# Kernel optimization log

Hardware: AMD Instinct MI355X
Metric: run time of the kernel (lower is better)

The kernel has to match this reference:

```python
import jax, jax.numpy as jnp
import numpy as np
import math

B, C_IN, C_QK, H, W, NH = 1, 256, 128, 96, 96, 8
SCALE = math.sqrt(C_QK / NH)  # sqrt(planes/num_head) = 4.0
TEMP = 1.0


def conv1x1(x, w, b=None):
    # x: [B, Cin, H, W], w: [Cout, Cin] -> [B, Cout, H, W]
    y = jnp.einsum('bchw,oc->bohw', x, w)
    if b is not None:
        y = y + b[None, :, None, None]
    return y


def maxpool2x2(x):
    return jax.lax.reduce_window(x, -jnp.inf, jax.lax.max,
                                 (1, 1, 2, 2), (1, 1, 2, 2), 'VALID')


def setup_inputs() -> dict:
    key = jax.random.key(0)
    ks = jax.random.split(key, 5)
    x = jax.random.normal(ks[0], (B, C_IN, H, W), dtype=jnp.float32)
    # conv weights: init.normal_(w, 0, 0.01), zero bias; conv_value has no bias
    w_q = jax.random.normal(ks[1], (C_QK, C_IN), dtype=jnp.float32) * 0.01
    b_q = jnp.zeros((C_QK,), dtype=jnp.float32)
    w_k = jax.random.normal(ks[2], (C_QK, C_IN), dtype=jnp.float32) * 0.01
    b_k = jnp.zeros((C_QK,), dtype=jnp.float32)
    w_v = jax.random.normal(ks[3], (C_IN, C_IN), dtype=jnp.float32) * 0.01
    return {'x': x, 'w_q': w_q, 'b_q': b_q, 'w_k': w_k, 'b_k': b_k, 'w_v': w_v}


def reference(x, w_q, b_q, w_k, b_k, w_v):
    residual = x
    input_x = maxpool2x2(x)                       # [B, Cin, H/2, W/2]
    Hd, Wd = H // 2, W // 2
    Nq, Nk = H * W, Hd * Wd

    q = conv1x1(x, w_q, b_q)                      # [B, Cqk, H, W]
    k = conv1x1(input_x, w_k, b_k)                # [B, Cqk, Hd, Wd]
    v = conv1x1(input_x, w_v)                     # [B, Cin, Hd, Wd]

    dq = C_QK // NH
    dv = C_IN // NH
    q = q.reshape(B * NH, dq, Nq)
    k = k.reshape(B * NH, dq, Nk)
    v = v.reshape(B * NH, dv, Nk)

    # dot distance: scaled by sqrt(planes/num_head) and temp (nowd empty)
    sim = jnp.einsum('bdq,bdk->bqk', q, k) / (SCALE * TEMP)
    attn = jax.nn.softmax(sim, axis=2)            # softmax over keys

    # out = value @ attn^T  -> [B*NH, dv, Nq]
    out = jnp.einsum('bdk,bqk->bdq', v, attn)
    out = out.reshape(B, C_IN, H, W)
    return out + residual
```

## Files before the change

kernel.cpp:

```cpp
#include <hip/hip_runtime.h>
#include <hip/hip_bf16.h>
#include <math.h>

#define C_IN   256
#define C_QK   128
#define NH     8
#define H_     96
#define W_     96
#define NQ     (H_*W_)
#define HD     48
#define WD     48
#define NK     (HD*WD)
#define DQ     16
#define DV     32
#define NQC    (NQ/32)
#define NKC    (NK/32)
#define KSTEPS (C_IN/16)
#define QS     0.3606737602222409f

typedef __attribute__((ext_vector_type(8)))  short short8v;
typedef __attribute__((ext_vector_type(16))) float f32x16;
typedef __attribute__((ext_vector_type(2)))  int   v2i;

union B8u { uint u[4]; short8v v; };

static __device__ inline ushort bf16r(float f) {
    __hip_bfloat16 h = __float2bfloat16(f);
    return *reinterpret_cast<ushort*>(&h);
}
static __device__ inline uint cvtpk(float lo, float hi) {
    uint r;
    asm("v_cvt_pk_bf16_f32 %0, %1, %2" : "=v"(r) : "v"(lo), "v"(hi));
    return r;
}
static __device__ inline void lswap(uint a, uint b, uint& x, uint& y, int hi) {
#if __has_builtin(__builtin_amdgcn_permlane32_swap)
    v2i r = __builtin_amdgcn_permlane32_swap((int)a, (int)b, false, false);
    x = (uint)r.x;
    y = (uint)r.y;
#else
    uint bx = (uint)__shfl_xor((int)b, 32);
    uint ax = (uint)__shfl_xor((int)a, 32);
    x = hi ? bx : a;
    y = hi ? b : ax;
#endif
}
static __device__ inline float fexp2(float v) {
#if __has_builtin(__builtin_amdgcn_exp2f)
    return __builtin_amdgcn_exp2f(v);
#else
    return __expf(v * 0.6931471805599453f);
#endif
}

#define U_XB   (NQC*KSTEPS*64)
#define U_XPB  (NKC*KSTEPS*64)
#define U_WQ   (4*KSTEPS*64)
#define U_WK   (4*KSTEPS*64)
#define U_WV   (8*KSTEPS*64)
#define U_FRAG (U_XB+U_XPB+U_WQ+U_WK+U_WV)
#define U_TOT  (U_FRAG + 128)

__global__ __launch_bounds__(256) void prep_kernel(
    const float* __restrict__ x,  const float* __restrict__ wq, const float* __restrict__ bq,
    const float* __restrict__ wk, const float* __restrict__ wv,
    ushort* __restrict__ xbP, ushort* __restrict__ xpbP,
    ushort* __restrict__ wqP, ushort* __restrict__ wkP, ushort* __restrict__ wvP,
    float* __restrict__ bqs)
{
    int t = blockIdx.x * 256 + threadIdx.x;
    if (t >= U_TOT) return;
    if (t >= U_FRAG) { int i = t - U_FRAG; bqs[i] = bq[i] * QS; return; }

    union { ushort s[8]; uint4 v; } ou;
    int u = t;
    if (u < U_XB) {
        int l = u & 63, rest = u >> 6;
        int ks = rest & 15, nc = rest >> 4;
        int n  = nc * 32 + (l & 31);
        int k0 = ks * 16 + 8 * (l >> 5);
        #pragma unroll
        for (int j = 0; j < 8; ++j) ou.s[j] = bf16r(x[(size_t)(k0 + j) * NQ + n]);
        *(uint4*)&xbP[(size_t)u * 8] = ou.v;
        return;
    }
    u -= U_XB;
    if (u < U_XPB) {
        int l = u & 63, rest = u >> 6;
        int ks = rest & 15, nc = rest >> 4;
        int np = nc * 32 + (l & 31);
        int k0 = ks * 16 + 8 * (l >> 5);
        int py = np / WD, px = np - py * WD;
        const float* base = x + (2 * py) * W_ + 2 * px;
        #pragma unroll
        for (int j = 0; j < 8; ++j) {
            const float* p = base + (size_t)(k0 + j) * NQ;
            ou.s[j] = bf16r(fmaxf(fmaxf(p[0], p[1]), fmaxf(p[W_], p[W_ + 1])));
        }
        *(uint4*)&xpbP[(size_t)u * 8] = ou.v;
        return;
    }
    u -= U_XPB;
    if (u < U_WQ) {
        int l = u & 63, ks = (u >> 6) & 15, mb = u >> 10;
        int m = mb * 32 + (l & 31), k0 = ks * 16 + 8 * (l >> 5);
        #pragma unroll
        for (int j = 0; j < 8; ++j) ou.s[j] = bf16r(wq[m * C_IN + k0 + j] * QS);
        *(uint4*)&wqP[(size_t)u * 8] = ou.v;
        return;
    }
    u -= U_WQ;
    if (u < U_WK) {
        int l = u & 63, ks = (u >> 6) & 15, mb = u >> 10;
        int m = mb * 32 + (l & 31), k0 = ks * 16 + 8 * (l >> 5);
        #pragma unroll
        for (int j = 0; j < 8; ++j) ou.s[j] = bf16r(wk[m * C_IN + k0 + j]);
        *(uint4*)&wkP[(size_t)u * 8] = ou.v;
        return;
    }
    u -= U_WK;
    {
        int l = u & 63, ks = (u >> 6) & 15, cb = u >> 10;
        int c = cb * 32 + (l & 31), k0 = ks * 16 + 8 * (l >> 5);
        #pragma unroll
        for (int j = 0; j < 8; ++j) ou.s[j] = bf16r(wv[c * C_IN + k0 + j]);
        *(uint4*)&wvP[(size_t)u * 8] = ou.v;
    }
}

static __device__ inline f32x16 mfma_loop(const ushort* __restrict__ A,
                                          const ushort* __restrict__ B) {
    f32x16 acc;
    #pragma unroll
    for (int r = 0; r < 16; ++r) acc[r] = 0.0f;
    #pragma unroll
    for (int s = 0; s < KSTEPS; ++s) {
        short8v a = *(const short8v*)(A + (size_t)s * 512);
        short8v b = *(const short8v*)(B + (size_t)s * 512);
        acc = __builtin_amdgcn_mfma_f32_32x32x16_bf16(a, b, acc, 0, 0, 0);
    }
    return acc;
}
static __device__ inline void xform(const f32x16& acc, int hi, short8v& F1, short8v& F2) {
    uint a0 = cvtpk(acc[0],  acc[1]),  a1 = cvtpk(acc[2],  acc[3]);
    uint b0 = cvtpk(acc[4],  acc[5]),  b1 = cvtpk(acc[6],  acc[7]);
    uint a2 = cvtpk(acc[8],  acc[9]),  a3 = cvtpk(acc[10], acc[11]);
    uint b2 = cvtpk(acc[12], acc[13]), b3 = cvtpk(acc[14], acc[15]);
    B8u f1, f2;
    lswap(a0, b0, f1.u[0], f1.u[2], hi);
    lswap(a1, b1, f1.u[1], f1.u[3], hi);
    lswap(a2, b2, f2.u[0], f2.u[2], hi);
    lswap(a3, b3, f2.u[1], f2.u[3], hi);
    F1 = f1.v; F2 = f2.v;
}

__global__ __launch_bounds__(256) void gemm_qk(const ushort* __restrict__ Wp,
                                               const ushort* __restrict__ Xp,
                                               const float* __restrict__ bias,
                                               ushort* __restrict__ outP, int NC) {
    int lane = threadIdx.x & 63, wvi = threadIdx.x >> 6;
    int hi = lane >> 5;
    int mb = blockIdx.x;
    int nc = blockIdx.y * 4 + wvi;
    const ushort* A = Wp + ((size_t)(mb * KSTEPS) * 64 + lane) * 8;
    const ushort* B = Xp + ((size_t)(nc * KSTEPS) * 64 + lane) * 8;
    f32x16 acc = mfma_loop(A, B);
    #pragma unroll
    for (int r = 0; r < 16; ++r)
        acc[r] += bias[mb * 32 + (r & 3) + 8 * (r >> 2) + 4 * hi];
    short8v F1, F2;
    xform(acc, hi, F1, F2);
    *(short8v*)&outP[((size_t)((2 * mb)     * NC + nc) * 64 + lane) * 8] = F1;
    *(short8v*)&outP[((size_t)((2 * mb + 1) * NC + nc) * 64 + lane) * 8] = F2;
}

__global__ __launch_bounds__(256) void gemm_v(const ushort* __restrict__ Xp,
                                              const ushort* __restrict__ Wvp,
                                              ushort* __restrict__ vpack) {
    int lane = threadIdx.x & 63, wvi = threadIdx.x >> 6;
    int hi = lane >> 5;
    int cb = blockIdx.x;
    int kc = blockIdx.y * 4 + wvi;
    const ushort* A = Xp  + ((size_t)(kc * KSTEPS) * 64 + lane) * 8;
    const ushort* B = Wvp + ((size_t)(cb * KSTEPS) * 64 + lane) * 8;
    f32x16 acc = mfma_loop(A, B);
    short8v F1, F2;
    xform(acc, hi, F1, F2);
    *(short8v*)&vpack[((size_t)((cb * NKC + kc) * 2 + 0) * 64 + lane) * 8] = F1;
    *(short8v*)&vpack[((size_t)((cb * NKC + kc) * 2 + 1) * 64 + lane) * 8] = F2;
}

__global__ __launch_bounds__(256) void attn_kernel(const ushort* __restrict__ qpack,
                                                   const ushort* __restrict__ kpack,
                                                   const ushort* __restrict__ vpack,
                                                   const float* __restrict__ x,
                                                   float* __restrict__ out) {
    __shared__ float comb[2 * 64 * 17];
    const int h = blockIdx.y;
    const int tid = threadIdx.x, lane = tid & 63;
    const int wvi = tid >> 6;
    const int qg = wvi & 1, kh = wvi >> 1;
    const int q31 = lane & 31, hi = lane >> 5;
    const int qc = blockIdx.x * 2 + qg;
    const int q = qc * 32 + q31;

    short8v qf = *(const short8v*)&qpack[((size_t)(h * NQC + qc) * 64 + lane) * 8];

    const ushort* kp = kpack + ((size_t)(h * NKC + kh * 36) * 64 + lane) * 8;
    const ushort* vp = vpack + ((size_t)(h * NKC + kh * 36) * 2 * 64 + lane) * 8;

    short8v kf = *(const short8v*)kp;
    short8v v0 = *(const short8v*)vp;
    short8v v1 = *(const short8v*)(vp + 512);

    f32x16 o, zc;
    #pragma unroll
    for (int r = 0; r < 16; ++r) { o[r] = 0.0f; zc[r] = 0.0f; }
    float rsum = 0.0f;

    #pragma unroll 2
    for (int c = 0; c < 36; ++c) {
        short8v kcur = kf, v0c = v0, v1c = v1;
        int cn = (c == 35) ? 0 : (c + 1);
        kf = *(const short8v*)(kp + (size_t)cn * 512);
        v0 = *(const short8v*)(vp + (size_t)cn * 1024);
        v1 = *(const short8v*)(vp + (size_t)cn * 1024 + 512);

        f32x16 s = __builtin_amdgcn_mfma_f32_32x32x16_bf16(kcur, qf, zc, 0, 0, 0);

        float e[16];
        #pragma unroll
        for (int r = 0; r < 16; ++r) e[r] = fexp2(s[r]);
        float t0 = 0.0f;
        #pragma unroll
        for (int r = 0; r < 16; ++r) t0 += e[r];
        rsum += t0;

        uint a0 = cvtpk(e[0],  e[1]),  a1 = cvtpk(e[2],  e[3]);
        uint b0 = cvtpk(e[4],  e[5]),  b1 = cvtpk(e[6],  e[7]);
        uint a2 = cvtpk(e[8],  e[9]),  a3 = cvtpk(e[10], e[11]);
        uint b2 = cvtpk(e[12], e[13]), b3 = cvtpk(e[14], e[15]);
        B8u B1, B2;
        lswap(a0, b0, B1.u[0], B1.u[2], hi);
        lswap(a1, b1, B1.u[1], B1.u[3], hi);
        lswap(a2, b2, B2.u[0], B2.u[2], hi);
        lswap(a3, b3, B2.u[1], B2.u[3], hi);

        o = __builtin_amdgcn_mfma_f32_32x32x16_bf16(v0c, B1.v, o, 0, 0, 0);
        o = __builtin_amdgcn_mfma_f32_32x32x16_bf16(v1c, B2.v, o, 0, 0, 0);
    }

    rsum += __shfl_xor(rsum, 32);

    if (kh == 1) {
        float* cb_ = &comb[(qg * 64 + lane) * 17];
        #pragma unroll
        for (int r = 0; r < 16; ++r) cb_[r] = o[r];
        cb_[16] = rsum;
    }
    __syncthreads();
    if (kh == 0) {
        const float* cb_ = &comb[(qg * 64 + lane) * 17];
        #pragma unroll
        for (int r = 0; r < 16; ++r) o[r] += cb_[r];
        float inv = 1.0f / (rsum + cb_[16]);
        #pragma unroll
        for (int r = 0; r < 16; ++r) {
            int dv = (r & 3) + 8 * (r >> 2) + 4 * hi;
            size_t i0 = (size_t)(h * DV + dv) * NQ + q;
            out[i0] = o[r] * inv + x[i0];
        }
    }
}

extern "C" void kernel_launch(void* const* d_in, const int* in_sizes, int n_in,
                              void* d_out, int out_size, void* d_ws, size_t ws_size,
                              hipStream_t stream) {
    const float* x  = (const float*)d_in[0];
    const float* wq = (const float*)d_in[1];
    const float* bq = (const float*)d_in[2];
    const float* wk = (const float*)d_in[3];
    const float* bk = (const float*)d_in[4];
    const float* wv = (const float*)d_in[5];
    float* out = (float*)d_out;

    ushort* p = (ushort*)d_ws;
    ushort* xbP   = p;  p += (size_t)U_XB  * 8;
    ushort* xpbP  = p;  p += (size_t)U_XPB * 8;
    ushort* wqP   = p;  p += (size_t)U_WQ  * 8;
    ushort* wkP   = p;  p += (size_t)U_WK  * 8;
    ushort* wvP   = p;  p += (size_t)U_WV  * 8;
    ushort* qpack = p;  p += (size_t)NH * NQC * 64 * 8;
    ushort* kpack = p;  p += (size_t)NH * NKC * 64 * 8;
    ushort* vpack = p;  p += (size_t)NH * NKC * 2 * 64 * 8;
    float*  bqs   = (float*)p;

    prep_kernel<<<(U_TOT + 255) / 256, 256, 0, stream>>>(x, wq, bq, wk, wv,
                                                         xbP, xpbP, wqP, wkP, wvP, bqs);
    gemm_qk<<<dim3(4, NQC / 4), 256, 0, stream>>>(wqP, xbP, bqs, qpack, NQC);
    gemm_qk<<<dim3(4, NKC / 4), 256, 0, stream>>>(wkP, xpbP, bk, kpack, NKC);
    gemm_v <<<dim3(NH, NKC / 4), 256, 0, stream>>>(xpbP, wvP, vpack);
    attn_kernel<<<dim3(NQC / 2, NH), 256, 0, stream>>>(qpack, kpack, vpack, x, out);
}
```

Baseline: 118.0 us.

## Fuse projection GEMMs into one launch and split attention keys four ways

The three separate projection GEMM launches (Q, K, V) are merged into one kernel that maps a flat tile index to the right sub-GEMM, which removes two launch gaps and lets the small K/V work share the machine with Q. The attention kernel now has each wave handle two query chunks against a quarter of the keys, so each K/V fragment load is reused across two queries. Partial outputs and row sums from all four waves are combined through shared memory. This costs more registers (launch bound of 4 blocks per SM hint) and a larger reduction step, and the grid keeps the same number of blocks.

```diff
diff --git a/kernel.cpp b/kernel.cpp
--- a/kernel.cpp
+++ b/kernel.cpp
@@ -15,6 +15,8 @@
 #define DV     32
 #define NQC    (NQ/32)
 #define NKC    (NK/32)
+#define QPAIRS (NQC/2)
+#define KQRT   (NKC/4)
 #define KSTEPS (C_IN/16)
 #define QS     0.3606737602222409f
 
@@ -154,116 +156,171 @@
     F1 = f1.v; F2 = f2.v;
 }
 
-__global__ __launch_bounds__(256) void gemm_qk(const ushort* __restrict__ Wp,
-                                               const ushort* __restrict__ Xp,
-                                               const float* __restrict__ bias,
-                                               ushort* __restrict__ outP, int NC) {
+#define T_Q 1152
+#define T_K (T_Q + 288)
+#define T_ALL (T_K + 576)
+
+__global__ __launch_bounds__(256) void gemm_fused(
+    const ushort* __restrict__ xbP, const ushort* __restrict__ xpbP,
+    const ushort* __restrict__ wqP, const ushort* __restrict__ wkP,
+    const ushort* __restrict__ wvP,
+    const float* __restrict__ bqs, const float* __restrict__ bk,
+    ushort* __restrict__ qpack, ushort* __restrict__ kpack, ushort* __restrict__ vpack)
+{
     int lane = threadIdx.x & 63, wvi = threadIdx.x >> 6;
     int hi = lane >> 5;
-    int mb = blockIdx.x;
-    int nc = blockIdx.y * 4 + wvi;
-    const ushort* A = Wp + ((size_t)(mb * KSTEPS) * 64 + lane) * 8;
-    const ushort* B = Xp + ((size_t)(nc * KSTEPS) * 64 + lane) * 8;
-    f32x16 acc = mfma_loop(A, B);
-    #pragma unroll
-    for (int r = 0; r < 16; ++r)
-        acc[r] += bias[mb * 32 + (r & 3) + 8 * (r >> 2) + 4 * hi];
-    short8v F1, F2;
-    xform(acc, hi, F1, F2);
-    *(short8v*)&outP[((size_t)((2 * mb)     * NC + nc) * 64 + lane) * 8] = F1;
-    *(short8v*)&outP[((size_t)((2 * mb + 1) * NC + nc) * 64 + lane) * 8] = F2;
-}
-
-__global__ __launch_bounds__(256) void gemm_v(const ushort* __restrict__ Xp,
-                                              const ushort* __restrict__ Wvp,
-                                              ushort* __restrict__ vpack) {
-    int lane = threadIdx.x & 63, wvi = threadIdx.x >> 6;
-    int hi = lane >> 5;
-    int cb = blockIdx.x;
-    int kc = blockIdx.y * 4 + wvi;
-    const ushort* A = Xp  + ((size_t)(kc * KSTEPS) * 64 + lane) * 8;
-    const ushort* B = Wvp + ((size_t)(cb * KSTEPS) * 64 + lane) * 8;
-    f32x16 acc = mfma_loop(A, B);
-    short8v F1, F2;
-    xform(acc, hi, F1, F2);
-    *(short8v*)&vpack[((size_t)((cb * NKC + kc) * 2 + 0) * 64 + lane) * 8] = F1;
-    *(short8v*)&vpack[((size_t)((cb * NKC + kc) * 2 + 1) * 64 + lane) * 8] = F2;
-}
-
-__global__ __launch_bounds__(256) void attn_kernel(const ushort* __restrict__ qpack,
-                                                   const ushort* __restrict__ kpack,
-                                                   const ushort* __restrict__ vpack,
-                                                   const float* __restrict__ x,
-                                                   float* __restrict__ out) {
-    __shared__ float comb[2 * 64 * 17];
+    int t = blockIdx.x * 4 + wvi;
+    if (t >= T_ALL) return;
+
+    if (t < T_Q) {
+        int mb = t / NQC, nc = t - mb * NQC;
+        const ushort* A = wqP + ((size_t)(mb * KSTEPS) * 64 + lane) * 8;
+        const ushort* B = xbP + ((size_t)(nc * KSTEPS) * 64 + lane) * 8;
+        f32x16 acc = mfma_loop(A, B);
+        #pragma unroll
+        for (int r = 0; r < 16; ++r)
+            acc[r] += bqs[mb * 32 + (r & 3) + 8 * (r >> 2) + 4 * hi];
+        short8v F1, F2;
+        xform(acc, hi, F1, F2);
+        *(short8v*)&qpack[((size_t)((2 * mb)     * NQC + nc) * 64 + lane) * 8] = F1;
+        *(short8v*)&qpack[((size_t)((2 * mb + 1) * NQC + nc) * 64 + lane) * 8] = F2;
+    } else if (t < T_K) {
+        int t2 = t - T_Q;
+        int mb = t2 / NKC, nc = t2 - mb * NKC;
+        const ushort* A = wkP  + ((size_t)(mb * KSTEPS) * 64 + lane) * 8;
+        const ushort* B = xpbP + ((size_t)(nc * KSTEPS) * 64 + lane) * 8;
+        f32x16 acc = mfma_loop(A, B);
+        #pragma unroll
+        for (int r = 0; r < 16; ++r)
+            acc[r] += bk[mb * 32 + (r & 3) + 8 * (r >> 2) + 4 * hi];
+        short8v F1, F2;
+        xform(acc, hi, F1, F2);
+        *(short8v*)&kpack[((size_t)((2 * mb)     * NKC + nc) * 64 + lane) * 8] = F1;
+        *(short8v*)&kpack[((size_t)((2 * mb + 1) * NKC + nc) * 64 + lane) * 8] = F2;
+    } else {
+        int t3 = t - T_K;
+        int cb = t3 / NKC, kc = t3 - cb * NKC;
+        const ushort* A = xpbP + ((size_t)(kc * KSTEPS) * 64 + lane) * 8;
+        const ushort* B = wvP  + ((size_t)(cb * KSTEPS) * 64 + lane) * 8;
+        f32x16 acc = mfma_loop(A, B);
+        short8v F1, F2;
+        xform(acc, hi, F1, F2);
+        *(short8v*)&vpack[((size_t)((cb * NKC + kc) * 2 + 0) * 64 + lane) * 8] = F1;
+        *(short8v*)&vpack[((size_t)((cb * NKC + kc) * 2 + 1) * 64 + lane) * 8] = F2;
+    }
+}
+
+__global__ __launch_bounds__(256, 4) void attn_kernel(const ushort* __restrict__ qpack,
+                                                      const ushort* __restrict__ kpack,
+                                                      const ushort* __restrict__ vpack,
+                                                      const float* __restrict__ x,
+                                                      float* __restrict__ out) {
+    __shared__ float part[4][2][64][20];
     const int h = blockIdx.y;
     const int tid = threadIdx.x, lane = tid & 63;
-    const int wvi = tid >> 6;
-    const int qg = wvi & 1, kh = wvi >> 1;
+    const int kh = tid >> 6;
     const int q31 = lane & 31, hi = lane >> 5;
-    const int qc = blockIdx.x * 2 + qg;
-    const int q = qc * 32 + q31;
-
-    short8v qf = *(const short8v*)&qpack[((size_t)(h * NQC + qc) * 64 + lane) * 8];
-
-    const ushort* kp = kpack + ((size_t)(h * NKC + kh * 36) * 64 + lane) * 8;
-    const ushort* vp = vpack + ((size_t)(h * NKC + kh * 36) * 2 * 64 + lane) * 8;
+    const int qp = blockIdx.x;
+
+    short8v qf0 = *(const short8v*)&qpack[((size_t)(h * NQC + 2 * qp)     * 64 + lane) * 8];
+    short8v qf1 = *(const short8v*)&qpack[((size_t)(h * NQC + 2 * qp + 1) * 64 + lane) * 8];
+
+    const ushort* kp = kpack + ((size_t)(h * NKC + kh * KQRT) * 64 + lane) * 8;
+    const ushort* vp = vpack + ((size_t)(h * NKC + kh * KQRT) * 2 * 64 + lane) * 8;
 
     short8v kf = *(const short8v*)kp;
     short8v v0 = *(const short8v*)vp;
     short8v v1 = *(const short8v*)(vp + 512);
 
-    f32x16 o, zc;
+    f32x16 o0, o1, zc;
     #pragma unroll
-    for (int r = 0; r < 16; ++r) { o[r] = 0.0f; zc[r] = 0.0f; }
-    float rsum = 0.0f;
-
-    #pragma unroll 2
-    for (int c = 0; c < 36; ++c) {
+    for (int r = 0; r < 16; ++r) { o0[r] = 0.0f; o1[r] = 0.0f; zc[r] = 0.0f; }
+    float rs0 = 0.0f, rs1 = 0.0f;
+
+    for (int c = 0; c < KQRT; ++c) {
         short8v kcur = kf, v0c = v0, v1c = v1;
-        int cn = (c == 35) ? 0 : (c + 1);
+        int cn = (c == KQRT - 1) ? 0 : (c + 1);
         kf = *(const short8v*)(kp + (size_t)cn * 512);
         v0 = *(const short8v*)(vp + (size_t)cn * 1024);
         v1 = *(const short8v*)(vp + (size_t)cn * 1024 + 512);
 
-        f32x16 s = __builtin_amdgcn_mfma_f32_32x32x16_bf16(kcur, qf, zc, 0, 0, 0);
-
-        float e[16];
-        #pragma unroll
-        for (int r = 0; r < 16; ++r) e[r] = fexp2(s[r]);
-        float t0 = 0.0f;
-        #pragma unroll
-        for (int r = 0; r < 16; ++r) t0 += e[r];
-        rsum += t0;
-
-        uint a0 = cvtpk(e[0],  e[1]),  a1 = cvtpk(e[2],  e[3]);
-        uint b0 = cvtpk(e[4],  e[5]),  b1 = cvtpk(e[6],  e[7]);
-        uint a2 = cvtpk(e[8],  e[9]),  a3 = cvtpk(e[10], e[11]);
-        uint b2 = cvtpk(e[12], e[13]), b3 = cvtpk(e[14], e[15]);
-        B8u B1, B2;
-        lswap(a0, b0, B1.u[0], B1.u[2], hi);
-        lswap(a1, b1, B1.u[1], B1.u[3], hi);
-        lswap(a2, b2, B2.u[0], B2.u[2], hi);
-        lswap(a3, b3, B2.u[1], B2.u[3], hi);
-
-        o = __builtin_amdgcn_mfma_f32_32x32x16_bf16(v0c, B1.v, o, 0, 0, 0);
-        o = __builtin_amdgcn_mfma_f32_32x32x16_bf16(v1c, B2.v, o, 0, 0, 0);
-    }
-
-    rsum += __shfl_xor(rsum, 32);
-
-    if (kh == 1) {
-        float* cb_ = &comb[(qg * 64 + lane) * 17];
-        #pragma unroll
-        for (int r = 0; r < 16; ++r) cb_[r] = o[r];
-        cb_[16] = rsum;
+        {
+            f32x16 s = __builtin_amdgcn_mfma_f32_32x32x16_bf16(kcur, qf0, zc, 0, 0, 0);
+            float e[16];
+            #pragma unroll
+            for (int r = 0; r < 16; ++r) e[r] = fexp2(s[r]);
+            float t0 = 0.0f;
+            #pragma unroll
+            for (int r = 0; r < 16; ++r) t0 += e[r];
+            rs0 += t0;
+            uint a0 = cvtpk(e[0],  e[1]),  a1 = cvtpk(e[2],  e[3]);
+            uint b0 = cvtpk(e[4],  e[5]),  b1 = cvtpk(e[6],  e[7]);
+            uint a2 = cvtpk(e[8],  e[9]),  a3 = cvtpk(e[10], e[11]);
+            uint b2 = cvtpk(e[12], e[13]), b3 = cvtpk(e[14], e[15]);
+            B8u B1, B2;
+            lswap(a0, b0, B1.u[0], B1.u[2], hi);
+            lswap(a1, b1, B1.u[1], B1.u[3], hi);
+            lswap(a2, b2, B2.u[0], B2.u[2], hi);
+            lswap(a3, b3, B2.u[1], B2.u[3], hi);
+            o0 = __builtin_amdgcn_mfma_f32_32x32x16_bf16(v0c, B1.v, o0, 0, 0, 0);
+            o0 = __builtin_amdgcn_mfma_f32_32x32x16_bf16(v1c, B2.v, o0, 0, 0, 0);
+        }
+        {
+            f32x16 s = __builtin_amdgcn_mfma_f32_32x32x16_bf16(kcur, qf1, zc, 0, 0, 0);
+            float e[16];
+            #pragma unroll
+            for (int r = 0; r < 16; ++r) e[r] = fexp2(s[r]);
+            float t0 = 0.0f;
+            #pragma unroll
+            for (int r = 0; r < 16; ++r) t0 += e[r];
+            rs1 += t0;
+            uint a0 = cvtpk(e[0],  e[1]),  a1 = cvtpk(e[2],  e[3]);
+            uint b0 = cvtpk(e[4],  e[5]),  b1 = cvtpk(e[6],  e[7]);
+            uint a2 = cvtpk(e[8],  e[9]),  a3 = cvtpk(e[10], e[11]);
+            uint b2 = cvtpk(e[12], e[13]), b3 = cvtpk(e[14], e[15]);
+            B8u B1, B2;
+            lswap(a0, b0, B1.u[0], B1.u[2], hi);
+            lswap(a1, b1, B1.u[1], B1.u[3], hi);
+            lswap(a2, b2, B2.u[0], B2.u[2], hi);
+            lswap(a3, b3, B2.u[1], B2.u[3], hi);
+            o1 = __builtin_amdgcn_mfma_f32_32x32x16_bf16(v0c, B1.v, o1, 0, 0, 0);
+            o1 = __builtin_amdgcn_mfma_f32_32x32x16_bf16(v1c, B2.v, o1, 0, 0, 0);
+        }
+    }
+
+    rs0 += __shfl_xor(rs0, 32);
+    rs1 += __shfl_xor(rs1, 32);
+
+    {
+        float* p0 = &part[kh][0][lane][0];
+        #pragma unroll
+        for (int i = 0; i < 4; ++i)
+            *(float4*)&p0[4 * i] = *(float4*)((const float*)&o0 + 4 * i);
+        p0[16] = rs0;
+        float* p1 = &part[kh][1][lane][0];
+        #pragma unroll
+        for (int i = 0; i < 4; ++i)
+            *(float4*)&p1[4 * i] = *(float4*)((const float*)&o1 + 4 * i);
+        p1[16] = rs1;
     }
     __syncthreads();
-    if (kh == 0) {
-        const float* cb_ = &comb[(qg * 64 + lane) * 17];
-        #pragma unroll
-        for (int r = 0; r < 16; ++r) o[r] += cb_[r];
-        float inv = 1.0f / (rsum + cb_[16]);
+
+    if (kh < 2) {
+        float o[16] = {};
+        float rs = 0.0f;
+        #pragma unroll
+        for (int w = 0; w < 4; ++w) {
+            const float* pw = &part[w][kh][lane][0];
+            #pragma unroll
+            for (int i = 0; i < 4; ++i) {
+                float4 f = *(const float4*)&pw[4 * i];
+                o[4 * i + 0] += f.x; o[4 * i + 1] += f.y;
+                o[4 * i + 2] += f.z; o[4 * i + 3] += f.w;
+            }
+            rs += pw[16];
+        }
+        float inv = 1.0f / rs;
+        int q = (2 * qp + kh) * 32 + q31;
         #pragma unroll
         for (int r = 0; r < 16; ++r) {
             int dv = (r & 3) + 8 * (r >> 2) + 4 * hi;
@@ -297,8 +354,7 @@
 
     prep_kernel<<<(U_TOT + 255) / 256, 256, 0, stream>>>(x, wq, bq, wk, wv,
                                                          xbP, xpbP, wqP, wkP, wvP, bqs);
-    gemm_qk<<<dim3(4, NQC / 4), 256, 0, stream>>>(wqP, xbP, bqs, qpack, NQC);
-    gemm_qk<<<dim3(4, NKC / 4), 256, 0, stream>>>(wkP, xpbP, bk, kpack, NKC);
-    gemm_v <<<dim3(NH, NKC / 4), 256, 0, stream>>>(xpbP, wvP, vpack);
-    attn_kernel<<<dim3(NQC / 2, NH), 256, 0, stream>>>(qpack, kpack, vpack, x, out);
-}
+    gemm_fused<<<(T_ALL + 3) / 4, 256, 0, stream>>>(xbP, xpbP, wqP, wkP, wvP,
+                                                    bqs, bk, qpack, kpack, vpack);
+    attn_kernel<<<dim3(QPAIRS, NH), 256, 0, stream>>>(qpack, kpack, vpack, x, out);
+}
```

Result: faster. 105.8 us (-10.3%).
